# Kernel optimization log

Hardware: AMD Instinct MI355X
Metric: run time of the kernel (lower is better)

Reference implementation:

```python
import jax, jax.numpy as jnp
import numpy as np

B, S, H = 4, 4096, 1024
GAMMA = 0.96875


def decay_mask(seq_len, gamma, dtype=jnp.float32):
    # D[i, j] = gamma**(i-j) for i >= j, else 0 (causal gamma-decay mask)
    i = jnp.arange(seq_len)[:, None]
    j = jnp.arange(seq_len)[None, :]
    exp = (i - j).astype(dtype)
    return jnp.where(i >= j, jnp.power(jnp.asarray(gamma, dtype), exp), jnp.zeros((), dtype))


def setup_inputs() -> dict:
    key = jax.random.key(0)
    ks = jax.random.split(key, 6)
    sc = 1.0 / np.sqrt(H)
    return {
        "x": jax.random.normal(ks[0], (B, S, H), dtype=jnp.float32),
        "Wq": jax.random.normal(ks[1], (H, H), dtype=jnp.float32) * sc,
        "bq": jax.random.normal(ks[2], (H,), dtype=jnp.float32) * 0.01,
        "Wk": jax.random.normal(ks[3], (H, H), dtype=jnp.float32) * sc,
        "bk": jax.random.normal(ks[4], (H,), dtype=jnp.float32) * 0.01,
        "Wv": jax.random.normal(ks[5], (H, H), dtype=jnp.float32) * sc,
    }


def reference(x, Wq, bq, Wk, bk, Wv):
    # Parallel representation of retention.
    seq_len = x.shape[1]
    q = jnp.einsum("bsh,oh->bso", x, Wq) + bq  # [B,S,H]
    k = jnp.einsum("bsh,oh->bso", x, Wk) + bk  # [B,S,H]
    v = jnp.einsum("bsh,oh->bso", x, Wv)       # [B,S,H]
    D = decay_mask(seq_len, GAMMA, x.dtype)     # [S,S]
    scores = jnp.einsum("bqh,bkh->bqk", q, k) * D[None]  # [B,S,S]
    return jnp.einsum("bqk,bkh->bqh", scores, v)
```

## Files before the change

### kernel.cpp

```cpp
#include <hip/hip_runtime.h>


typedef __attribute__((ext_vector_type(8))) short short8;
typedef __attribute__((ext_vector_type(4))) float floatx4;

#define MFMA(a, b, c) __builtin_amdgcn_mfma_f32_16x16x32_bf16((a), (b), (c), 0, 0, 0)

#define B_SZ   4
#define S_LEN  4096
#define H_DIM  1024
#define NROWS  (B_SZ * S_LEN)
#define HP     1088
#define LOG2G  (-0.045803690f)

__device__ __forceinline__ unsigned short f32_to_bf16_rn(float f) {
    unsigned int u = __float_as_uint(f);
    u += 0x7FFFu + ((u >> 16) & 1u);
    return (unsigned short)(u >> 16);
}

#define GLOAD_LDS16(gptr, lptr)                                                        \
    __builtin_amdgcn_global_load_lds((__attribute__((address_space(1))) void*)(gptr),  \
                                     (__attribute__((address_space(3))) void*)(lptr),  \
                                     16, 0, 0)

#define BAR()                                   \
    do {                                        \
        asm volatile("" ::: "memory");          \
        __builtin_amdgcn_s_barrier();           \
        asm volatile("" ::: "memory");          \
    } while (0)

__device__ __forceinline__ void cvt_bf16_body(int i, const float* __restrict__ src,
                                              unsigned short* __restrict__ dst, int n4) {
    if (i >= n4) return;
    float4 v = ((const float4*)src)[i];
    ushort4 o;
    o.x = f32_to_bf16_rn(v.x);
    o.y = f32_to_bf16_rn(v.y);
    o.z = f32_to_bf16_rn(v.z);
    o.w = f32_to_bf16_rn(v.w);
    ((ushort4*)dst)[i] = o;
}

__device__ __forceinline__ void cvt_x_body(int idx, const float* __restrict__ src,
                                           unsigned short* __restrict__ dst) {
    int row = idx >> 7, c8 = (idx & 127) * 8;
    const float4* s = (const float4*)(src + (size_t)row * H_DIM + c8);
    float4 a = s[0], b = s[1];
    ushort4 o0, o1;
    o0.x = f32_to_bf16_rn(a.x); o0.y = f32_to_bf16_rn(a.y);
    o0.z = f32_to_bf16_rn(a.z); o0.w = f32_to_bf16_rn(a.w);
    o1.x = f32_to_bf16_rn(b.x); o1.y = f32_to_bf16_rn(b.y);
    o1.z = f32_to_bf16_rn(b.z); o1.w = f32_to_bf16_rn(b.w);
    ushort4* d = (ushort4*)(dst + (size_t)row * HP + c8);
    d[0] = o0; d[1] = o1;
}

__device__ __forceinline__ void fill_pad_body(int idx, unsigned short* __restrict__ dst) {
    int row = idx >> 3, c = idx & 7;
    uint4 v; v.x = (c == 0) ? 0x00003F80u : 0u; v.y = 0u; v.z = 0u; v.w = 0u;
    *(uint4*)(dst + (size_t)row * HP + 1024 + c * 8) = v;
}

__device__ __forceinline__ void zero_pb_body(int idx, unsigned short* __restrict__ pb) {
    int r = idx >> 13;
    int rem = idx & 8191;
    int row = rem >> 5, c8 = (rem & 31) * 8;
    int batch = r / 3, sub = r % 3;
    int qt = batch * 16 + (sub == 2 ? 1 : 0);
    int col0 = (sub == 2 ? 0 : sub * 256);
    uint4 z; z.x = 0u; z.y = 0u; z.z = 0u; z.w = 0u;
    *(uint4*)(pb + (size_t)qt * (256 * 768) + (size_t)row * 768 + col0 + c8) = z;
}

__device__ __forceinline__ void tr_cvt_body(float (&Lt)[128][33],
                                            const float* __restrict__ Wsrc,
                                            const float* __restrict__ bias,
                                            unsigned short* __restrict__ dst,
                                            int bx, int by, int tid) {
    if (by >= 32) {
        if (bx != 0) return;
        const int h0 = by * 32;
#pragma unroll
        for (int i = 0; i < 128; ++i) {
            int idx = i * 256 + tid;
            int r = idx >> 10, cc = idx & 1023;
            int h = h0 + r;
            float v = (h == 1024) ? bias[cc] : 0.0f;
            dst[(size_t)h * 1024 + cc] = f32_to_bf16_rn(v);
        }
        return;
    }
    const int w0 = bx * 128, h0 = by * 32;
#pragma unroll
    for (int i = 0; i < 16; ++i) {
        int idx = i * 256 + tid;
        int r = idx >> 5, cc = idx & 31;
        Lt[r][cc] = Wsrc[(size_t)(w0 + r) * 1024 + h0 + cc];
    }
    __syncthreads();
#pragma unroll
    for (int i = 0; i < 16; ++i) {
        int idx = i * 256 + tid;
        int hh = idx >> 7, ww = idx & 127;
        dst[(size_t)(h0 + hh) * 1024 + w0 + ww] = f32_to_bf16_rn(Lt[ww][hh]);
    }
}

__device__ __forceinline__ void gemm_body128(unsigned short (&As)[2][128 * 32],
                                             unsigned short (&Bs)[2][128 * 32],
                                             int bx, int by,
                                             const unsigned short* __restrict__ A, int lda,
                                             const unsigned short* __restrict__ W, int ldw,
                                             unsigned short* __restrict__ outp, int ldo,
                                             int K, int p0) {
    const int tid  = threadIdx.x;
    const int lane = tid & 63;
    const int w4   = tid >> 6;
    const int wm   = w4 >> 1, wn = w4 & 1;
    const int l15  = lane & 15;
    const int q8   = (lane >> 4) * 8;
    const int q4   = (lane >> 4) * 4;

    const int aRow0 = by * 128, wRow0 = bx * 128;

    floatx4 acc[4][4];
#pragma unroll
    for (int i = 0; i < 4; ++i)
#pragma unroll
        for (int j = 0; j < 4; ++j) acc[i][j] = (floatx4)0.0f;

    for (int k0 = 0; k0 < K; k0 += 64) {
        __syncthreads();
#pragma unroll
        for (int p = 0; p < 2; ++p) {
            const int c = p * 256 + tid;
            const unsigned short* gA = A + (size_t)(aRow0 + (c >> 2)) * lda + k0 + (c & 3) * 8;
            const unsigned short* gW = W + (size_t)(wRow0 + (c >> 2)) * ldw + k0 + (c & 3) * 8;
            char* dA0 = (char*)&As[0][0] + (size_t)(p * 256 + w4 * 64) * 16;
            char* dA1 = (char*)&As[1][0] + (size_t)(p * 256 + w4 * 64) * 16;
            char* dB0 = (char*)&Bs[0][0] + (size_t)(p * 256 + w4 * 64) * 16;
            char* dB1 = (char*)&Bs[1][0] + (size_t)(p * 256 + w4 * 64) * 16;
            GLOAD_LDS16(gA,      dA0);
            GLOAD_LDS16(gA + 32, dA1);
            GLOAD_LDS16(gW,      dB0);
            GLOAD_LDS16(gW + 32, dB1);
        }
        __syncthreads();

#pragma unroll
        for (int h = 0; h < 2; ++h) {
            short8 af[4], bf[4];
#pragma unroll
            for (int mt = 0; mt < 4; ++mt)
                af[mt] = *(const short8*)(&As[h][0] + (wm * 64 + mt * 16 + l15) * 32 + q8);
#pragma unroll
            for (int nt = 0; nt < 4; ++nt)
                bf[nt] = *(const short8*)(&Bs[h][0] + (wn * 64 + nt * 16 + l15) * 32 + q8);
#pragma unroll
            for (int mt = 0; mt < 4; ++mt)
#pragma unroll
                for (int nt = 0; nt < 4; ++nt)
                    acc[mt][nt] = MFMA(af[mt], bf[nt], acc[mt][nt]);
        }
    }

#pragma unroll
    for (int nt = 0; nt < 4; ++nt) {
        const int ol = wn * 64 + nt * 16 + l15;
#pragma unroll
        for (int mt = 0; mt < 4; ++mt) {
#pragma unroll
            for (int r = 0; r < 4; ++r) {
                const int nl = wm * 64 + mt * 16 + q4 + r;
                const int o = wRow0 + ol;
                if (o < p0)
                    outp[(size_t)(aRow0 + nl) * ldo + o] = f32_to_bf16_rn(acc[mt][nt][r]);
            }
        }
    }
}

template <int MODE, int NS>
__device__ __forceinline__ void g256_body(unsigned short (&lds)[4][2][8192],
                                          int bx, int by,
                                          const unsigned short* __restrict__ Abase, int lda,
                                          const unsigned short* __restrict__ Wbase, int ldw,
                                          void* __restrict__ outp) {
    const int tid  = threadIdx.x;
    const int lane = tid & 63;
    const int wv   = tid >> 6;
    const int wm   = wv >> 2, wn = wv & 3;
    const int l15  = lane & 15;
    const int q    = lane >> 4;
    const int q4   = q * 4;

    const unsigned short* Ap;
    const unsigned short* Wp;
    int ql = 0;
    if (MODE == 0) {
        Ap = Abase + (size_t)(by * 256) * lda;
        Wp = Wbase + (size_t)(bx * 256) * ldw;
    } else if (MODE == 1) {
        Ap = Abase + (size_t)(bx * 256) * lda;
        Wp = Wbase + (size_t)(by * 256) * ldw;
    } else if (MODE == 2) {
        ql = by & 15;
        const int j256 = ql - 2 + bx;
        if (j256 < 0) return;
        Ap = Abase + (size_t)(by * 256) * lda;
        Wp = Wbase + (size_t)((by >> 4) * S_LEN + j256 * 256) * ldw;
    } else {
        ql = by & 15;
        Ap = Abase + (size_t)by * (256 * 768);
        Wp = Wbase + ((ptrdiff_t)((by >> 4) * H_DIM + bx * 256)) * S_LEN
                   + ((ptrdiff_t)ql - 2) * 256;
    }

    int arow[2], ach[2];
#pragma unroll
    for (int i = 0; i < 2; ++i) {
        int c  = i * 512 + tid;
        arow[i] = c >> 2;
        ach[i]  = (((c & 3) ^ ((c >> 3) & 3))) * 8;
    }

    floatx4 acc[8][4];
#pragma unroll
    for (int i = 0; i < 8; ++i)
#pragma unroll
        for (int j = 0; j < 4; ++j) acc[i][j] = (floatx4)0.0f;

    auto STAGE = [&](int ks) {
        const int sl = ks & 3;
        const int kc = ks * 32;
        char* da = (char*)&lds[sl][0][0] + (size_t)(wv * 64) * 16;
        char* db = (char*)&lds[sl][1][0] + (size_t)(wv * 64) * 16;
#pragma unroll
        for (int i = 0; i < 2; ++i) {
            GLOAD_LDS16(Ap + (size_t)arow[i] * lda + kc + ach[i], da + i * 8192);
            GLOAD_LDS16(Wp + (size_t)arow[i] * ldw + kc + ach[i], db + i * 8192);
        }
    };

    auto COMPUTE = [&](int ks) {
        const int sl = ks & 3;
        const unsigned short* Asl = &lds[sl][0][0];
        const unsigned short* Bsl = &lds[sl][1][0];
        short8 af[8], bf[4];
#pragma unroll
        for (int mt = 0; mt < 8; ++mt) {
            const int row = wm * 128 + mt * 16 + l15;
            af[mt] = *(const short8*)(Asl + row * 32 + ((q ^ ((row >> 1) & 3)) * 8));
        }
#pragma unroll
        for (int nt = 0; nt < 4; ++nt) {
            const int row = wn * 64 + nt * 16 + l15;
            bf[nt] = *(const short8*)(Bsl + row * 32 + ((q ^ ((row >> 1) & 3)) * 8));
        }
        __builtin_amdgcn_s_setprio(1);
#pragma unroll
        for (int mt = 0; mt < 8; ++mt)
#pragma unroll
            for (int nt = 0; nt < 4; ++nt)
                acc[mt][nt] = MFMA(af[mt], bf[nt], acc[mt][nt]);
        __builtin_amdgcn_s_setprio(0);
    };

    STAGE(0); STAGE(1); STAGE(2);

    int ks = 0;
#pragma unroll 1
    for (; ks < NS - 3; ++ks) {
        STAGE(ks + 3);
        asm volatile("s_waitcnt vmcnt(12)" ::: "memory");
        BAR();
        COMPUTE(ks);
        BAR();
    }
    asm volatile("s_waitcnt vmcnt(8)" ::: "memory");
    BAR();
    COMPUTE(ks);
    BAR();
    asm volatile("s_waitcnt vmcnt(4)" ::: "memory");
    BAR();
    COMPUTE(ks + 1);
    BAR();
    asm volatile("s_waitcnt vmcnt(0)" ::: "memory");
    BAR();
    COMPUTE(ks + 2);

#pragma unroll
    for (int nt = 0; nt < 4; ++nt) {
        const int ol = wn * 64 + nt * 16 + l15;
#pragma unroll
        for (int mt = 0; mt < 8; ++mt) {
#pragma unroll
            for (int r = 0; r < 4; ++r) {
                const int nl = wm * 128 + mt * 16 + q4 + r;
                const float v = acc[mt][nt][r];
                if (MODE == 0) {
                    const int o = bx * 256 + ol;
                    if (o < HP)
                        ((unsigned short*)outp)[(size_t)(by * 256 + nl) * HP + o] =
                            f32_to_bf16_rn(v);
                } else if (MODE == 1) {
                    const int s  = by * 256 + ol;
                    const int hh = bx * 256 + nl;
                    ((unsigned short*)outp)[((size_t)(s >> 12) * H_DIM + hh) * S_LEN +
                                            (s & (S_LEN - 1))] = f32_to_bf16_rn(v);
                } else if (MODE == 2) {
                    const int d = (2 - bx) * 256 + nl - ol;
                    const float pv = (d >= 0) ? v * exp2f((float)d * LOG2G) : 0.0f;
                    ((unsigned short*)outp)[(size_t)by * (256 * 768) + (size_t)nl * 768 +
                                            bx * 256 + ol] = f32_to_bf16_rn(pv);
                } else {
                    ((float*)outp)[(size_t)(by * 256 + nl) * H_DIM + bx * 256 + ol] = v;
                }
            }
        }
    }
}

__global__ __launch_bounds__(256) void prep_small(const float* __restrict__ Wq,
                                                  const float* __restrict__ bq,
                                                  const float* __restrict__ Wk,
                                                  const float* __restrict__ bk,
                                                  const float* __restrict__ Wv,
                                                  unsigned short* __restrict__ wqT,
                                                  unsigned short* __restrict__ wkT,
                                                  unsigned short* __restrict__ wvb,
                                                  unsigned short* __restrict__ pb,
                                                  unsigned short* __restrict__ xtb) {
    __shared__ float Lt[128][33];
    const int t = blockIdx.x, tid = threadIdx.x;
    if (t < 288) {
        tr_cvt_body(Lt, Wq, bq, wqT, t & 7, t >> 3, tid);
    } else if (t < 608) {
        const int t2 = t - 288;
        tr_cvt_body(Lt, Wk, bk, wkT, t2 & 7, t2 >> 3, tid);
    } else if (t < 1632) {
        cvt_bf16_body((t - 608) * 256 + tid, Wv, wvb, H_DIM * H_DIM / 4);
    } else if (t < 2016) {
        zero_pb_body((t - 1632) * 256 + tid, pb);
    } else {
        fill_pad_body((t - 2016) * 256 + tid, xtb);
    }
}

__global__ __launch_bounds__(256) void cvtx_p1(const float* __restrict__ x,
                                               unsigned short* __restrict__ xtb,
                                               const unsigned short* __restrict__ wkT,
                                               const unsigned short* __restrict__ wqT,
                                               unsigned short* __restrict__ p1) {
    __shared__ unsigned short As[2][128 * 32];
    __shared__ unsigned short Bs[2][128 * 32];
    const int t = blockIdx.x;
    if (t < 90) {
        gemm_body128(As, Bs, t % 9, t / 9, wkT, 1024, wqT, 1024, p1, HP, 1024, HP);
    } else {
        cvt_x_body((t - 90) * 256 + threadIdx.x, x, xtb);
    }
}

__global__ __launch_bounds__(512, 2) void g256_g(const unsigned short* __restrict__ xtb,
                                                 const unsigned short* __restrict__ p1,
                                                 unsigned short* __restrict__ gb) {
    __shared__ unsigned short lds[4][2][8192];
    const int bid = blockIdx.x;
    const int g = bid & 7, j = bid >> 3;
    g256_body<0, 34>(lds, j % 5, g * 8 + j / 5, xtb, HP, p1, HP, gb);
}

__global__ __launch_bounds__(512, 2) void g256_pbvt(const unsigned short* __restrict__ gb,
                                                    const unsigned short* __restrict__ xtb,
                                                    const unsigned short* __restrict__ wvb,
                                                    unsigned short* __restrict__ pb,
                                                    unsigned short* __restrict__ vtb) {
    __shared__ unsigned short lds[4][2][8192];
    const int t = blockIdx.x;
    if (t < 192) {
        const int g = t & 7, j = t >> 3;
        g256_body<2, 34>(lds, j % 3, g * 8 + j / 3, gb, HP, xtb, HP, pb);
    } else {
        const int t2 = t - 192;
        const int g = t2 & 7, j = t2 >> 3;
        g256_body<1, 32>(lds, j & 3, g * 8 + (j >> 2), wvb, 1024, xtb, HP, vtb);
    }
}

__global__ __launch_bounds__(512, 2) void g256_out(const unsigned short* __restrict__ pb,
                                                   const unsigned short* __restrict__ vtb,
                                                   float* __restrict__ out) {
    __shared__ unsigned short lds[4][2][8192];
    const int bid = blockIdx.x;
    const int g = bid & 7, j = bid >> 3;
    g256_body<3, 24>(lds, j & 3, g * 8 + (j >> 2), pb, 768, vtb, S_LEN, out);
}

extern "C" void kernel_launch(void* const* d_in, const int* in_sizes, int n_in,
                              void* d_out, int out_size, void* d_ws, size_t ws_size,
                              hipStream_t stream) {
    (void)in_sizes; (void)n_in; (void)out_size; (void)ws_size;

    const float* x  = (const float*)d_in[0];
    const float* Wq = (const float*)d_in[1];
    const float* bq = (const float*)d_in[2];
    const float* Wk = (const float*)d_in[3];
    const float* bk = (const float*)d_in[4];
    const float* Wv = (const float*)d_in[5];
    float* out = (float*)d_out;

    unsigned short* xtb = (unsigned short*)d_ws;
    unsigned short* gb  = xtb + (size_t)NROWS * HP;
    unsigned short* vtb = gb  + (size_t)NROWS * HP;
    unsigned short* pb  = vtb + (size_t)NROWS * H_DIM;
    unsigned short* wqT = pb  + (size_t)64 * 256 * 768;
    unsigned short* wkT = wqT + (size_t)1152 * 1024;
    unsigned short* p1  = wkT + (size_t)1280 * 1024;
    unsigned short* wvb = p1  + (size_t)1280 * HP;

    prep_small<<<2528, 256, 0, stream>>>(Wq, bq, Wk, bk, Wv, wqT, wkT, wvb, pb, xtb);
    cvtx_p1<<<90 + 8192, 256, 0, stream>>>(x, xtb, wkT, wqT, p1);
    g256_g<<<320, 512, 0, stream>>>(xtb, p1, gb);
    g256_pbvt<<<192 + 256, 512, 0, stream>>>(gb, xtb, wvb, pb, vtb);
    g256_out<<<256, 512, 0, stream>>>(pb, vtb, out);
}
```

Before: 330.3 us.

## Restructure 256-tile GEMM into K=64 double-buffered pipeline with quadrant MFMA interleave

Replaces the 4-stage K=32 LDS ring with a 2-stage K=64 double buffer and splits each tile step into four quadrant phases. LDS fragment reads and MFMAs alternate between phases, and the next tile's B half is issued mid-iteration. The aim is to halve loop iterations, widen each load, and overlap global-to-LDS traffic with MFMA work at a finer grain. In exchange it adds many more barriers per iteration and leaves only one tile of prefetch lookahead, so memory latency may be less well hidden.

```diff
diff --git a/kernel.cpp b/kernel.cpp
--- a/kernel.cpp
+++ b/kernel.cpp
@@ -182,8 +182,8 @@
     }
 }
 
-template <int MODE, int NS>
-__device__ __forceinline__ void g256_body(unsigned short (&lds)[4][2][8192],
+template <int MODE, int NT>
+__device__ __forceinline__ void g256_body(unsigned short (&lds)[2][2][16384],
                                           int bx, int by,
                                           const unsigned short* __restrict__ Abase, int lda,
                                           const unsigned short* __restrict__ Wbase, int ldw,
@@ -218,78 +218,97 @@
                    + ((ptrdiff_t)ql - 2) * 256;
     }
 
-    int arow[2], ach[2];
-#pragma unroll
-    for (int i = 0; i < 2; ++i) {
-        int c  = i * 512 + tid;
-        arow[i] = c >> 2;
-        ach[i]  = (((c & 3) ^ ((c >> 3) & 3))) * 8;
-    }
-
     floatx4 acc[8][4];
 #pragma unroll
     for (int i = 0; i < 8; ++i)
 #pragma unroll
         for (int j = 0; j < 4; ++j) acc[i][j] = (floatx4)0.0f;
 
-    auto STAGE = [&](int ks) {
-        const int sl = ks & 3;
-        const int kc = ks * 32;
-        char* da = (char*)&lds[sl][0][0] + (size_t)(wv * 64) * 16;
-        char* db = (char*)&lds[sl][1][0] + (size_t)(wv * 64) * 16;
-#pragma unroll
-        for (int i = 0; i < 2; ++i) {
-            GLOAD_LDS16(Ap + (size_t)arow[i] * lda + kc + ach[i], da + i * 8192);
-            GLOAD_LDS16(Wp + (size_t)arow[i] * ldw + kc + ach[i], db + i * 8192);
+    auto STAGE2 = [&](int t, int m) {
+        const int b  = t & 1;
+        const int k0 = t * 64;
+        const unsigned short* gp = m ? Wp : Ap;
+        const int ld = m ? ldw : lda;
+        char* base = (char*)&lds[b][m][0];
+#pragma unroll
+        for (int i = 0; i < 4; ++i) {
+            const int c   = i * 512 + tid;
+            const int row = c >> 3;
+            const int ch  = (c & 7) ^ (row & 7);
+            GLOAD_LDS16(gp + (size_t)row * ld + k0 + ch * 8,
+                        base + (size_t)(i * 512 + wv * 64) * 16);
         }
     };
 
-    auto COMPUTE = [&](int ks) {
-        const int sl = ks & 3;
-        const unsigned short* Asl = &lds[sl][0][0];
-        const unsigned short* Bsl = &lds[sl][1][0];
-        short8 af[8], bf[4];
-#pragma unroll
-        for (int mt = 0; mt < 8; ++mt) {
-            const int row = wm * 128 + mt * 16 + l15;
-            af[mt] = *(const short8*)(Asl + row * 32 + ((q ^ ((row >> 1) & 3)) * 8));
-        }
-#pragma unroll
-        for (int nt = 0; nt < 4; ++nt) {
-            const int row = wn * 64 + nt * 16 + l15;
-            bf[nt] = *(const short8*)(Bsl + row * 32 + ((q ^ ((row >> 1) & 3)) * 8));
-        }
+    short8 afr[4][2], bfr[2][2];
+    auto RDA = [&](int t, int mh) {
+        const unsigned short* base = &lds[t & 1][0][0];
+#pragma unroll
+        for (int mt = 0; mt < 4; ++mt) {
+            const int r = wm * 128 + mh * 64 + mt * 16 + l15;
+#pragma unroll
+            for (int h = 0; h < 2; ++h) {
+                const int ch = (h * 4 + q) ^ (r & 7);
+                afr[mt][h] = *(const short8*)(base + r * 64 + ch * 8);
+            }
+        }
+    };
+    auto RDB = [&](int t, int nh) {
+        const unsigned short* base = &lds[t & 1][1][0];
+#pragma unroll
+        for (int nt = 0; nt < 2; ++nt) {
+            const int r = wn * 64 + (nh * 2 + nt) * 16 + l15;
+#pragma unroll
+            for (int h = 0; h < 2; ++h) {
+                const int ch = (h * 4 + q) ^ (r & 7);
+                bfr[nt][h] = *(const short8*)(base + r * 64 + ch * 8);
+            }
+        }
+    };
+    auto QMFMA = [&](int mh, int nh) {
         __builtin_amdgcn_s_setprio(1);
 #pragma unroll
-        for (int mt = 0; mt < 8; ++mt)
-#pragma unroll
-            for (int nt = 0; nt < 4; ++nt)
-                acc[mt][nt] = MFMA(af[mt], bf[nt], acc[mt][nt]);
+        for (int mt = 0; mt < 4; ++mt)
+#pragma unroll
+            for (int nt = 0; nt < 2; ++nt)
+#pragma unroll
+                for (int h = 0; h < 2; ++h)
+                    acc[mh * 4 + mt][nh * 2 + nt] =
+                        MFMA(afr[mt][h], bfr[nt][h], acc[mh * 4 + mt][nh * 2 + nt]);
         __builtin_amdgcn_s_setprio(0);
     };
 
-    STAGE(0); STAGE(1); STAGE(2);
-
-    int ks = 0;
+    STAGE2(0, 0);
+    STAGE2(0, 1);
+
 #pragma unroll 1
-    for (; ks < NS - 3; ++ks) {
-        STAGE(ks + 3);
-        asm volatile("s_waitcnt vmcnt(12)" ::: "memory");
-        BAR();
-        COMPUTE(ks);
-        BAR();
-    }
-    asm volatile("s_waitcnt vmcnt(8)" ::: "memory");
-    BAR();
-    COMPUTE(ks);
-    BAR();
-    asm volatile("s_waitcnt vmcnt(4)" ::: "memory");
-    BAR();
-    COMPUTE(ks + 1);
-    BAR();
-    asm volatile("s_waitcnt vmcnt(0)" ::: "memory");
-    BAR();
-    COMPUTE(ks + 2);
+    for (int t = 0; t < NT; ++t) {
+        if (t + 1 < NT) {
+            STAGE2(t + 1, 0);
+            asm volatile("s_waitcnt vmcnt(4)" ::: "memory");
+        } else {
+            asm volatile("s_waitcnt vmcnt(0)" ::: "memory");
+        }
+        BAR();
+        RDA(t, 0);
+        RDB(t, 0);
+        BAR();
+        QMFMA(0, 0);
+        BAR();
+        if (t + 1 < NT) STAGE2(t + 1, 1);
+        RDB(t, 1);
+        BAR();
+        QMFMA(0, 1);
+        BAR();
+        RDA(t, 1);
+        BAR();
+        QMFMA(1, 1);
+        BAR();
+        RDB(t, 0);
+        BAR();
+        QMFMA(1, 0);
+        BAR();
+    }
 
 #pragma unroll
     for (int nt = 0; nt < 4; ++nt) {
@@ -367,10 +386,10 @@
 __global__ __launch_bounds__(512, 2) void g256_g(const unsigned short* __restrict__ xtb,
                                                  const unsigned short* __restrict__ p1,
                                                  unsigned short* __restrict__ gb) {
-    __shared__ unsigned short lds[4][2][8192];
+    __shared__ unsigned short lds[2][2][16384];
     const int bid = blockIdx.x;
     const int g = bid & 7, j = bid >> 3;
-    g256_body<0, 34>(lds, j % 5, g * 8 + j / 5, xtb, HP, p1, HP, gb);
+    g256_body<0, 17>(lds, j % 5, g * 8 + j / 5, xtb, HP, p1, HP, gb);
 }
 
 __global__ __launch_bounds__(512, 2) void g256_pbvt(const unsigned short* __restrict__ gb,
@@ -378,25 +397,25 @@
                                                     const unsigned short* __restrict__ wvb,
                                                     unsigned short* __restrict__ pb,
                                                     unsigned short* __restrict__ vtb) {
-    __shared__ unsigned short lds[4][2][8192];
+    __shared__ unsigned short lds[2][2][16384];
     const int t = blockIdx.x;
     if (t < 192) {
         const int g = t & 7, j = t >> 3;
-        g256_body<2, 34>(lds, j % 3, g * 8 + j / 3, gb, HP, xtb, HP, pb);
+        g256_body<2, 17>(lds, j % 3, g * 8 + j / 3, gb, HP, xtb, HP, pb);
     } else {
         const int t2 = t - 192;
         const int g = t2 & 7, j = t2 >> 3;
-        g256_body<1, 32>(lds, j & 3, g * 8 + (j >> 2), wvb, 1024, xtb, HP, vtb);
+        g256_body<1, 16>(lds, j & 3, g * 8 + (j >> 2), wvb, 1024, xtb, HP, vtb);
     }
 }
 
 __global__ __launch_bounds__(512, 2) void g256_out(const unsigned short* __restrict__ pb,
                                                    const unsigned short* __restrict__ vtb,
                                                    float* __restrict__ out) {
-    __shared__ unsigned short lds[4][2][8192];
+    __shared__ unsigned short lds[2][2][16384];
     const int bid = blockIdx.x;
     const int g = bid & 7, j = bid >> 3;
-    g256_body<3, 24>(lds, j & 3, g * 8 + (j >> 2), pb, 768, vtb, S_LEN, out);
+    g256_body<3, 12>(lds, j & 3, g * 8 + (j >> 2), pb, 768, vtb, S_LEN, out);
 }
 
 extern "C" void kernel_launch(void* const* d_in, const int* in_sizes, int n_in,
```

Measured after the change: 329.8 us. Within noise of the previous version (-0.1%).
